# Kernel optimization log

Hardware: AMD Instinct MI355X
Metric: run time of the kernel (lower is better)

## Reference

```python
import jax, jax.numpy as jnp
import numpy as np

C = 256
B, H, W = 8, 192, 192

def _xavier(key, shape):
    fan_in, fan_out = shape[1], shape[0]
    limit = float(np.sqrt(6.0 / (fan_in + fan_out)))
    return jax.random.uniform(key, shape, jnp.float32, -limit, limit)

def setup_inputs() -> dict:
    key = jax.random.key(0)
    ks = jax.random.split(key, 9)
    return {
        'query': jax.random.normal(ks[0], (B, C, H, W), jnp.float32),
        'key':   jax.random.normal(ks[1], (B, C, H, W), jnp.float32),
        'value': jax.random.normal(ks[2], (B, C, H, W), jnp.float32),
        'Wq': _xavier(ks[3], (C, C)), 'bq': jnp.zeros((C,), jnp.float32),
        'Wk': _xavier(ks[4], (C, C)), 'bk': jnp.zeros((C,), jnp.float32),
        'Wv': _xavier(ks[5], (C, C)), 'bv': jnp.zeros((C,), jnp.float32),
    }

def _conv1x1(x, Wm, b):
    # 1x1 conv == channel-mixing GEMM: [B,C,H,W] -> [B,C,H,W]
    return jnp.einsum('oi,bihw->bohw', Wm, x) + b[None, :, None, None]

def reference(query, key, value, Wq, bq, Wk, bk, Wv, bv):
    q = _conv1x1(query, Wq, bq)   # [B,C,H,W]
    k = _conv1x1(key, Wk, bk)
    v = _conv1x1(value, Wv, bv)
    # scores[b,c,h,h'] = sum_w q[b,c,h,w] * k[b,c,h',w]
    scores = jnp.einsum('bchw,bcgw->bchg', q, k)  # [B,C,H,H]
    attn = jax.nn.softmax(scores, axis=-1)
    out = jnp.einsum('bchg,bcgw->bchw', attn, v)  # [B,C,H,W]
    return out
```

## Files before the change

kernel.cpp:

```cpp
#include <hip/hip_runtime.h>
#include <hip/hip_bf16.h>

typedef _Float16 f16;
typedef f16   f16x8 __attribute__((ext_vector_type(8)));
typedef float f32x4 __attribute__((ext_vector_type(4)));

#define HW 36864
#define TS 9437184

__device__ __forceinline__ void gload16(const void* g, void* lds) {
  __builtin_amdgcn_global_load_lds(
      (const __attribute__((address_space(1))) unsigned int*)g,
      (__attribute__((address_space(3))) unsigned int*)lds, 16, 0, 0);
}

__global__ __launch_bounds__(256) void convert_w_kernel(
    const float* __restrict__ wq, const float* __restrict__ wk,
    const float* __restrict__ wv, f16* __restrict__ wp) {
  int i = blockIdx.x * 256 + threadIdx.x;
  wp[i]             = (f16)wq[i];
  wp[65536 + i]     = (f16)wk[i];
  wp[2 * 65536 + i] = (f16)wv[i];
}

__global__ __launch_bounds__(512) void conv1x1_kernel(
    const float* __restrict__ xq, const float* __restrict__ xk, const float* __restrict__ xv,
    const f16* __restrict__ wp,
    const float* __restrict__ bq, const float* __restrict__ bk, const float* __restrict__ bv,
    f16* __restrict__ qkv) {
  const int bid   = blockIdx.x;
  const int bt    = bid >> 5;
  const int strip = bid & 31;
  const int b     = bt / 3;
  const int t     = bt % 3;
  const float* __restrict__ in   = ((t == 0) ? xq : (t == 1 ? xk : xv)) + (size_t)b * TS;
  const float* __restrict__ bias = (t == 0) ? bq : (t == 1 ? bk : bv);
  const f16* __restrict__ W = wp + t * 65536;
  f16* __restrict__ outp    = qkv + (size_t)(b * 3 + t) * TS;

  const int tid = threadIdx.x;
  const int l   = tid & 63;
  const int wv  = tid >> 6;
  const int lr  = l & 15, lg = l >> 4;

  __shared__ __align__(16) float Xbuf[2][16384];

  const int fnp = wv & 1;
  const int foq = wv >> 1;

  float bz[4][4];
#pragma unroll
  for (int ff = 0; ff < 4; ++ff)
#pragma unroll
    for (int r = 0; r < 4; ++r) bz[ff][r] = bias[(foq * 4 + ff) * 16 + lg * 4 + r];

  auto ISSUE = [&](int tile, int bufi) {
    const int n0 = (strip * 18 + tile) * 64;
#pragma unroll
    for (int jj = 0; jj < 8; ++jj) {
      const int m   = wv * 8 + jj;
      const int i0  = m * 4 + (l >> 4);
      const int col = 4 * ((l & 15) ^ (((m >> 1) & 3) << 1));
      gload16(in + (size_t)i0 * HW + n0 + col, (char*)&Xbuf[bufi][0] + m * 1024);
    }
  };

  ISSUE(0, 0);
  __syncthreads();

  int cur = 0;
  for (int it = 0; it < 18; ++it) {
    if (it < 17) ISSUE(it + 1, cur ^ 1);

    const float* __restrict__ Xc = &Xbuf[cur][0];
    const int n0 = (strip * 18 + it) * 64;

    f32x4 acc[4][2];
#pragma unroll
    for (int ff = 0; ff < 4; ++ff)
#pragma unroll
      for (int e = 0; e < 2; ++e) acc[ff][e] = (f32x4){0.f, 0.f, 0.f, 0.f};

#pragma unroll
    for (int ks = 0; ks < 8; ++ks) {
      f16x8 bx[2];
#pragma unroll
      for (int e = 0; e < 2; ++e) {
        const int nc = lr + 16 * (fnp * 2 + e);
        union { f16 h[8]; f16x8 v; } u;
#pragma unroll
        for (int j = 0; j < 8; ++j)
          u.h[j] = (f16)Xc[(ks * 32 + lg * 8 + j) * 64 + (nc ^ (lg * 8))];
        bx[e] = u.v;
      }
      f16x8 aw[4];
#pragma unroll
      for (int ff = 0; ff < 4; ++ff)
        aw[ff] = *(const f16x8*)(W + ((foq * 4 + ff) * 16 + lr) * 256 + ks * 32 + lg * 8);
#pragma unroll
      for (int ff = 0; ff < 4; ++ff)
#pragma unroll
        for (int e = 0; e < 2; ++e)
          acc[ff][e] = __builtin_amdgcn_mfma_f32_16x16x32_f16(aw[ff], bx[e], acc[ff][e], 0, 0, 0);
    }

#pragma unroll
    for (int ff = 0; ff < 4; ++ff) {
      const int orow = (foq * 4 + ff) * 16 + lg * 4;
#pragma unroll
      for (int e = 0; e < 2; ++e)
#pragma unroll
        for (int r = 0; r < 4; ++r)
          outp[(size_t)(orow + r) * HW + n0 + (fnp * 2 + e) * 16 + lr] =
              (f16)(acc[ff][e][r] + bz[ff][r]);
    }

    __syncthreads();
    cur ^= 1;
  }
}

__global__ __launch_bounds__(768) void attn_kernel(
    const f16* __restrict__ qkv, float* __restrict__ outb) {
  const int c2  = blockIdx.x;
  const int b   = c2 >> 8;
  const int c   = c2 & 255;
  const int tid = threadIdx.x;
  const int l   = tid & 63;
  const int wv  = tid >> 6;
  const int lr  = l & 15, lg = l >> 4;

  const f16* __restrict__ qb = qkv + (size_t)(b * 3) * TS;
  const f16* __restrict__ q = qb + (size_t)c * HW;
  const f16* __restrict__ k = qb + (size_t)TS + (size_t)c * HW;
  const f16* __restrict__ v = qb + 2 * (size_t)TS + (size_t)c * HW;
  float* __restrict__ outc = outb + (size_t)b * TS + (size_t)c * HW;

  __shared__ f16 KA[192][200];
  __shared__ f16 Pf[192][200];

  const int h0 = wv * 16;

  f16x8 aq[6];
#pragma unroll
  for (int ks = 0; ks < 6; ++ks)
    aq[ks] = *(const f16x8*)(q + (h0 + lr) * 192 + ks * 32 + lg * 8);

  const int gA = (tid % 24) * 8, wA = (tid / 24) * 4;
  const int jB = tid + 768;
  const int gB = (jB % 24) * 8, wB = (jB / 24) * 4;
  uint2 vpA[8], vpB[8];
#pragma unroll
  for (int j = 0; j < 8; ++j) vpA[j] = *(const uint2*)(v + (gA + j) * 192 + wA);
  if (tid < 384) {
#pragma unroll
    for (int j = 0; j < 8; ++j) vpB[j] = *(const uint2*)(v + (gB + j) * 192 + wB);
  }

#pragma unroll
  for (int jj = 0; jj < 6; ++jj) {
    int id = tid + jj * 768;
    int g = id / 24, wo = id % 24;
    *(f16x8*)&KA[g][wo * 8] = *(const f16x8*)(k + g * 192 + wo * 8);
  }
  __syncthreads();

  {
    f32x4 S[12];
#pragma unroll
    for (int fg = 0; fg < 12; ++fg) S[fg] = (f32x4){0.f, 0.f, 0.f, 0.f};
#pragma unroll
    for (int ks = 0; ks < 6; ++ks)
#pragma unroll
      for (int fg = 0; fg < 12; ++fg) {
        f16x8 bk_ = *(const f16x8*)&KA[16 * fg + lr][ks * 32 + lg * 8];
        S[fg] = __builtin_amdgcn_mfma_f32_16x16x32_f16(aq[ks], bk_, S[fg], 0, 0, 0);
      }

#pragma unroll
    for (int r = 0; r < 4; ++r) {
      float m = S[0][r];
#pragma unroll
      for (int fg = 1; fg < 12; ++fg) m = fmaxf(m, S[fg][r]);
      m = fmaxf(m, __shfl_xor(m, 1));
      m = fmaxf(m, __shfl_xor(m, 2));
      m = fmaxf(m, __shfl_xor(m, 4));
      m = fmaxf(m, __shfl_xor(m, 8));
      float s = 0.f;
#pragma unroll
      for (int fg = 0; fg < 12; ++fg) {
        float e = __expf(S[fg][r] - m);
        S[fg][r] = e;
        s += e;
      }
      s += __shfl_xor(s, 1);
      s += __shfl_xor(s, 2);
      s += __shfl_xor(s, 4);
      s += __shfl_xor(s, 8);
      float rs = 1.f / s;
#pragma unroll
      for (int fg = 0; fg < 12; ++fg)
        Pf[h0 + lg * 4 + r][16 * fg + lr] = (f16)(S[fg][r] * rs);
    }
  }
  __syncthreads();

  {
#pragma unroll
    for (int qd = 0; qd < 4; ++qd) {
      union { unsigned short s[8]; f16x8 vec; } u;
#pragma unroll
      for (int j = 0; j < 8; ++j) u.s[j] = ((const unsigned short*)&vpA[j])[qd];
      *(f16x8*)&KA[wA + qd][gA] = u.vec;
    }
    if (tid < 384) {
#pragma unroll
      for (int qd = 0; qd < 4; ++qd) {
        union { unsigned short s[8]; f16x8 vec; } u;
#pragma unroll
        for (int j = 0; j < 8; ++j) u.s[j] = ((const unsigned short*)&vpB[j])[qd];
        *(f16x8*)&KA[wB + qd][gB] = u.vec;
      }
    }
  }
  __syncthreads();

  {
    f32x4 O[12];
#pragma unroll
    for (int fn = 0; fn < 12; ++fn) O[fn] = (f32x4){0.f, 0.f, 0.f, 0.f};

#pragma unroll
    for (int ks = 0; ks < 6; ++ks) {
      f16x8 pa = *(const f16x8*)&Pf[h0 + lr][ks * 32 + lg * 8];
#pragma unroll
      for (int fn = 0; fn < 12; ++fn) {
        f16x8 bv_ = *(const f16x8*)&KA[16 * fn + lr][ks * 32 + lg * 8];
        O[fn] = __builtin_amdgcn_mfma_f32_16x16x32_f16(pa, bv_, O[fn], 0, 0, 0);
      }
    }

#pragma unroll
    for (int fn = 0; fn < 12; ++fn)
#pragma unroll
      for (int r = 0; r < 4; ++r)
        outc[(size_t)(h0 + lg * 4 + r) * 192 + 16 * fn + lr] = O[fn][r];
  }
}

extern "C" void kernel_launch(void* const* d_in, const int* in_sizes, int n_in,
                              void* d_out, int out_size, void* d_ws, size_t ws_size,
                              hipStream_t stream) {
  const float* query = (const float*)d_in[0];
  const float* key_  = (const float*)d_in[1];
  const float* value = (const float*)d_in[2];
  const float* Wq    = (const float*)d_in[3];
  const float* bq    = (const float*)d_in[4];
  const float* Wk    = (const float*)d_in[5];
  const float* bk    = (const float*)d_in[6];
  const float* Wv    = (const float*)d_in[7];
  const float* bv    = (const float*)d_in[8];
  float* out = (float*)d_out;

  f16* wp  = (f16*)d_ws;
  f16* qkv = (f16*)((char*)d_ws + 524288);

  convert_w_kernel<<<256, 256, 0, stream>>>(Wq, Wk, Wv, wp);

  const size_t need_fused = 524288 + (size_t)8 * 3 * TS * 2;
  if (ws_size >= need_fused) {
    conv1x1_kernel<<<32 * 3 * 8, 512, 0, stream>>>(
        query, key_, value, wp, bq, bk, bv, qkv);
    attn_kernel<<<2048, 768, 0, stream>>>(qkv, out);
  } else {
    for (int b = 0; b < 8; ++b) {
      const size_t off = (size_t)b * TS;
      conv1x1_kernel<<<32 * 3, 512, 0, stream>>>(
          query + off, key_ + off, value + off, wp, bq, bk, bv, qkv);
      attn_kernel<<<256, 768, 0, stream>>>(qkv, out + off);
    }
  }
}
```

Baseline: 503.4 us.

## Stage conv input as swizzled fp16 in LDS and flatten tile scheduling

The 1x1-conv kernel now loads fp32 input tiles into registers, converts them to fp16 once, and stores them transposed into a swizzled LDS layout. Each MFMA B operand then becomes a single 16-byte LDS read, replacing eight scalar fp32 reads and conversions per operand. LDS use drops from 128 KB to 64 KB per block. The grid becomes 512 persistent-style blocks that each walk 27 flat tiles across batch and q/k/v, with a launch-bounds occupancy hint. In exchange, prefetch now goes through registers instead of direct global-to-LDS loads, and the bias is re-read from global memory at every store.

```diff
diff --git a/kernel.cpp b/kernel.cpp
--- a/kernel.cpp
+++ b/kernel.cpp
@@ -7,12 +7,6 @@
 
 #define HW 36864
 #define TS 9437184
-
-__device__ __forceinline__ void gload16(const void* g, void* lds) {
-  __builtin_amdgcn_global_load_lds(
-      (const __attribute__((address_space(1))) unsigned int*)g,
-      (__attribute__((address_space(3))) unsigned int*)lds, 16, 0, 0);
-}
 
 __global__ __launch_bounds__(256) void convert_w_kernel(
     const float* __restrict__ wq, const float* __restrict__ wk,
@@ -23,57 +17,72 @@
   wp[2 * 65536 + i] = (f16)wv[i];
 }
 
-__global__ __launch_bounds__(512) void conv1x1_kernel(
+__global__ __launch_bounds__(512, 4) void conv1x1_kernel(
     const float* __restrict__ xq, const float* __restrict__ xk, const float* __restrict__ xv,
     const f16* __restrict__ wp,
     const float* __restrict__ bq, const float* __restrict__ bk, const float* __restrict__ bv,
     f16* __restrict__ qkv) {
-  const int bid   = blockIdx.x;
-  const int bt    = bid >> 5;
-  const int strip = bid & 31;
-  const int b     = bt / 3;
-  const int t     = bt % 3;
-  const float* __restrict__ in   = ((t == 0) ? xq : (t == 1 ? xk : xv)) + (size_t)b * TS;
-  const float* __restrict__ bias = (t == 0) ? bq : (t == 1 ? bk : bv);
-  const f16* __restrict__ W = wp + t * 65536;
-  f16* __restrict__ outp    = qkv + (size_t)(b * 3 + t) * TS;
-
   const int tid = threadIdx.x;
   const int l   = tid & 63;
   const int wv  = tid >> 6;
   const int lr  = l & 15, lg = l >> 4;
-
-  __shared__ __align__(16) float Xbuf[2][16384];
-
   const int fnp = wv & 1;
   const int foq = wv >> 1;
 
-  float bz[4][4];
-#pragma unroll
-  for (int ff = 0; ff < 4; ++ff)
-#pragma unroll
-    for (int r = 0; r < 4; ++r) bz[ff][r] = bias[(foq * 4 + ff) * 16 + lg * 4 + r];
-
-  auto ISSUE = [&](int tile, int bufi) {
-    const int n0 = (strip * 18 + tile) * 64;
-#pragma unroll
-    for (int jj = 0; jj < 8; ++jj) {
-      const int m   = wv * 8 + jj;
-      const int i0  = m * 4 + (l >> 4);
-      const int col = 4 * ((l & 15) ^ (((m >> 1) & 3) << 1));
-      gload16(in + (size_t)i0 * HW + n0 + col, (char*)&Xbuf[bufi][0] + m * 1024);
-    }
+  __shared__ __align__(16) char Y[2][32768];
+
+  const int a   = tid & 63;
+  const int nb0 = tid >> 6;
+  const int tg0 = blockIdx.x * 27;
+
+  float4 rv[8];
+
+  auto ISSUE = [&](int tg) {
+    const int bt = tg / 576, tl = tg - bt * 576;
+    const int b = bt / 3, t = bt - b * 3;
+    const float* __restrict__ in =
+        ((t == 0) ? xq : (t == 1 ? xk : xv)) + (size_t)b * TS;
+    const int n0 = tl * 64;
+    const int i0 = 4 * a;
+#pragma unroll
+    for (int j = 0; j < 4; ++j)
+      rv[j] = *(const float4*)(in + (size_t)(i0 + j) * HW + n0 + 4 * nb0);
+#pragma unroll
+    for (int j = 0; j < 4; ++j)
+      rv[4 + j] = *(const float4*)(in + (size_t)(i0 + j) * HW + n0 + 4 * (nb0 + 8));
   };
 
-  ISSUE(0, 0);
+  auto COMMIT = [&](int bufi) {
+    char* bp = Y[bufi];
+#pragma unroll
+    for (int J = 0; J < 2; ++J) {
+#pragma unroll
+      for (int d = 0; d < 4; ++d) {
+        const int n = 4 * (nb0 + 8 * J) + d;
+        union { f16 h[4]; unsigned long long u; } p;
+#pragma unroll
+        for (int j = 0; j < 4; ++j) p.h[j] = (f16)((&rv[4 * J + j].x)[d]);
+        *(unsigned long long*)(bp + n * 512 + (((a >> 1) ^ (n & 7)) << 4) + ((a & 1) << 3)) = p.u;
+      }
+    }
+  };
+
+  ISSUE(tg0);
+  COMMIT(0);
   __syncthreads();
 
   int cur = 0;
-  for (int it = 0; it < 18; ++it) {
-    if (it < 17) ISSUE(it + 1, cur ^ 1);
-
-    const float* __restrict__ Xc = &Xbuf[cur][0];
-    const int n0 = (strip * 18 + it) * 64;
+  for (int tt = 0; tt < 27; ++tt) {
+    const int tg = tg0 + tt;
+    if (tt < 26) ISSUE(tg + 1);
+
+    const int bt = tg / 576, tl = tg - bt * 576;
+    const int b = bt / 3, t = bt - b * 3;
+    const f16* __restrict__ W = wp + t * 65536;
+    const float* __restrict__ bias = (t == 0) ? bq : (t == 1 ? bk : bv);
+    f16* __restrict__ outp = qkv + (size_t)(b * 3 + t) * TS;
+    const int n0 = tl * 64;
+    const char* __restrict__ Yc = Y[cur];
 
     f32x4 acc[4][2];
 #pragma unroll
@@ -86,12 +95,8 @@
       f16x8 bx[2];
 #pragma unroll
       for (int e = 0; e < 2; ++e) {
-        const int nc = lr + 16 * (fnp * 2 + e);
-        union { f16 h[8]; f16x8 v; } u;
-#pragma unroll
-        for (int j = 0; j < 8; ++j)
-          u.h[j] = (f16)Xc[(ks * 32 + lg * 8 + j) * 64 + (nc ^ (lg * 8))];
-        bx[e] = u.v;
+        const int n = lr + 16 * (2 * fnp + e);
+        bx[e] = *(const f16x8*)(Yc + n * 512 + (((4 * ks + lg) ^ (n & 7)) << 4));
       }
       f16x8 aw[4];
 #pragma unroll
@@ -106,15 +111,17 @@
 
 #pragma unroll
     for (int ff = 0; ff < 4; ++ff) {
-      const int orow = (foq * 4 + ff) * 16 + lg * 4;
-#pragma unroll
-      for (int e = 0; e < 2; ++e)
+      const int orow = foq * 64 + ff * 16 + lg * 4;
+#pragma unroll
+      for (int e = 0; e < 2; ++e) {
+        const int n = n0 + 16 * (2 * fnp + e) + lr;
 #pragma unroll
         for (int r = 0; r < 4; ++r)
-          outp[(size_t)(orow + r) * HW + n0 + (fnp * 2 + e) * 16 + lr] =
-              (f16)(acc[ff][e][r] + bz[ff][r]);
-    }
-
+          outp[(size_t)(orow + r) * HW + n] = (f16)(acc[ff][e][r] + bias[orow + r]);
+      }
+    }
+
+    if (tt < 26) COMMIT(cur ^ 1);
     __syncthreads();
     cur ^= 1;
   }
@@ -269,13 +276,13 @@
 
   const size_t need_fused = 524288 + (size_t)8 * 3 * TS * 2;
   if (ws_size >= need_fused) {
-    conv1x1_kernel<<<32 * 3 * 8, 512, 0, stream>>>(
+    conv1x1_kernel<<<512, 512, 0, stream>>>(
         query, key_, value, wp, bq, bk, bv, qkv);
     attn_kernel<<<2048, 768, 0, stream>>>(qkv, out);
   } else {
     for (int b = 0; b < 8; ++b) {
       const size_t off = (size_t)b * TS;
-      conv1x1_kernel<<<32 * 3, 512, 0, stream>>>(
+      conv1x1_kernel<<<64, 512, 0, stream>>>(
           query + off, key_ + off, value + off, wp, bq, bk, bv, qkv);
       attn_kernel<<<256, 768, 0, stream>>>(qkv, out + off);
     }
```

Result: slower. 926.9 us (+84.1%).

## Triple-buffer conv1x1 input halves with two-deep prefetch and counted waits

Applied to the files above, without the earlier changes.

The conv1x1 kernel now splits each 64-column tile's 256-channel reduction into two 128-channel halves. Halves rotate through three 32 KB LDS buffers, with two halves in flight ahead of compute. Plain __syncthreads is replaced with explicit s_waitcnt vmcnt counts plus raw s_barrier and sched_barrier fences, so the wait covers only the oldest pending half-tile rather than draining everything. This is meant to keep more global loads in flight and cut per-tile stall time, while also reducing total LDS use. The trade-off is a dependence on hand-managed vmcnt accounting: the output stores also count against vmcnt, which may force extra waiting.

```diff
diff --git a/kernel.cpp b/kernel.cpp
--- a/kernel.cpp
+++ b/kernel.cpp
@@ -43,7 +43,7 @@
   const int wv  = tid >> 6;
   const int lr  = l & 15, lg = l >> 4;
 
-  __shared__ __align__(16) float Xbuf[2][16384];
+  __shared__ __align__(16) float Xbuf[3][8192];
 
   const int fnp = wv & 1;
   const int foq = wv >> 1;
@@ -54,35 +54,44 @@
 #pragma unroll
     for (int r = 0; r < 4; ++r) bz[ff][r] = bias[(foq * 4 + ff) * 16 + lg * 4 + r];
 
-  auto ISSUE = [&](int tile, int bufi) {
-    const int n0 = (strip * 18 + tile) * 64;
-#pragma unroll
-    for (int jj = 0; jj < 8; ++jj) {
-      const int m   = wv * 8 + jj;
-      const int i0  = m * 4 + (l >> 4);
-      const int col = 4 * ((l & 15) ^ (((m >> 1) & 3) << 1));
-      gload16(in + (size_t)i0 * HW + n0 + col, (char*)&Xbuf[bufi][0] + m * 1024);
+  auto ISSUE = [&](int ht) {
+    const int bufi = ht % 3;
+    const int n0 = (strip * 18 + (ht >> 1)) * 64;
+    const int ib = (ht & 1) << 7;
+#pragma unroll
+    for (int jj = 0; jj < 4; ++jj) {
+      const int m    = wv * 4 + jj;
+      const int iloc = m * 4 + (l >> 4);
+      const int col  = 4 * ((l & 15) ^ (((m >> 1) & 3) << 1));
+      gload16(in + (size_t)(ib + iloc) * HW + n0 + col,
+              (char*)&Xbuf[bufi][0] + m * 1024);
     }
   };
 
-  ISSUE(0, 0);
-  __syncthreads();
-
-  int cur = 0;
-  for (int it = 0; it < 18; ++it) {
-    if (it < 17) ISSUE(it + 1, cur ^ 1);
-
-    const float* __restrict__ Xc = &Xbuf[cur][0];
-    const int n0 = (strip * 18 + it) * 64;
-
-    f32x4 acc[4][2];
-#pragma unroll
-    for (int ff = 0; ff < 4; ++ff)
-#pragma unroll
-      for (int e = 0; e < 2; ++e) acc[ff][e] = (f32x4){0.f, 0.f, 0.f, 0.f};
-
-#pragma unroll
-    for (int ks = 0; ks < 8; ++ks) {
+  ISSUE(0);
+  ISSUE(1);
+  asm volatile("s_waitcnt vmcnt(4)" ::: "memory");
+  __builtin_amdgcn_sched_barrier(0);
+  __builtin_amdgcn_s_barrier();
+  __builtin_amdgcn_sched_barrier(0);
+
+  f32x4 acc[4][2];
+#pragma unroll
+  for (int ff = 0; ff < 4; ++ff)
+#pragma unroll
+    for (int e = 0; e < 2; ++e) acc[ff][e] = (f32x4){0.f, 0.f, 0.f, 0.f};
+
+  for (int ht = 0; ht < 36; ++ht) {
+    if (ht + 2 < 36) {
+      ISSUE(ht + 2);
+      __builtin_amdgcn_sched_barrier(0);
+    }
+
+    const float* __restrict__ Xc = &Xbuf[ht % 3][0];
+    const int ihw = (ht & 1) * 128;
+
+#pragma unroll
+    for (int ks = 0; ks < 4; ++ks) {
       f16x8 bx[2];
 #pragma unroll
       for (int e = 0; e < 2; ++e) {
@@ -90,13 +99,13 @@
         union { f16 h[8]; f16x8 v; } u;
 #pragma unroll
         for (int j = 0; j < 8; ++j)
-          u.h[j] = (f16)Xc[(ks * 32 + lg * 8 + j) * 64 + (nc ^ (lg * 8))];
+          u.h[j] = (f16)Xc[(ks * 32 + lg * 8 + j) * 64 + (nc ^ (8 * lg))];
         bx[e] = u.v;
       }
       f16x8 aw[4];
 #pragma unroll
       for (int ff = 0; ff < 4; ++ff)
-        aw[ff] = *(const f16x8*)(W + ((foq * 4 + ff) * 16 + lr) * 256 + ks * 32 + lg * 8);
+        aw[ff] = *(const f16x8*)(W + ((foq * 4 + ff) * 16 + lr) * 256 + ihw + ks * 32 + lg * 8);
 #pragma unroll
       for (int ff = 0; ff < 4; ++ff)
 #pragma unroll
@@ -104,19 +113,32 @@
           acc[ff][e] = __builtin_amdgcn_mfma_f32_16x16x32_f16(aw[ff], bx[e], acc[ff][e], 0, 0, 0);
     }
 
-#pragma unroll
-    for (int ff = 0; ff < 4; ++ff) {
-      const int orow = (foq * 4 + ff) * 16 + lg * 4;
-#pragma unroll
-      for (int e = 0; e < 2; ++e)
-#pragma unroll
-        for (int r = 0; r < 4; ++r)
-          outp[(size_t)(orow + r) * HW + n0 + (fnp * 2 + e) * 16 + lr] =
-              (f16)(acc[ff][e][r] + bz[ff][r]);
-    }
-
-    __syncthreads();
-    cur ^= 1;
+    if (ht & 1) {
+      const int n0 = (strip * 18 + (ht >> 1)) * 64;
+#pragma unroll
+      for (int ff = 0; ff < 4; ++ff) {
+        const int orow = (foq * 4 + ff) * 16 + lg * 4;
+#pragma unroll
+        for (int e = 0; e < 2; ++e)
+#pragma unroll
+          for (int r = 0; r < 4; ++r)
+            outp[(size_t)(orow + r) * HW + n0 + (fnp * 2 + e) * 16 + lr] =
+                (f16)(acc[ff][e][r] + bz[ff][r]);
+#pragma unroll
+        for (int e = 0; e < 2; ++e) acc[ff][e] = (f32x4){0.f, 0.f, 0.f, 0.f};
+      }
+    }
+
+    if (ht + 2 < 36) {
+      asm volatile("s_waitcnt vmcnt(4)" ::: "memory");
+    } else if (ht + 1 < 36) {
+      asm volatile("s_waitcnt vmcnt(0)" ::: "memory");
+    }
+    if (ht + 1 < 36) {
+      __builtin_amdgcn_sched_barrier(0);
+      __builtin_amdgcn_s_barrier();
+      __builtin_amdgcn_sched_barrier(0);
+    }
   }
 }
 
```

New measurement: 778.1 us. +54.6%, slower.
